# Kernel tuning notes

Hardware: AMD Instinct MI355X
Metric: run time of the kernel (lower is better)

## Reference

```python
import jax, jax.numpy as jnp
import numpy as np

B, N, D, H = 16, 1024, 384, 6
DH = D // H  # 64 per-head dim


def _layernorm(x, w, b, eps=1e-5):
    mu = jnp.mean(x, axis=-1, keepdims=True)
    var = jnp.var(x, axis=-1, keepdims=True)
    return (x - mu) * jax.lax.rsqrt(var + eps) * w + b


def setup_inputs() -> dict:
    key = jax.random.key(0)
    ks = jax.random.split(key, 10)
    std = 0.02
    return {
        "X": jax.random.normal(ks[0], (B, N, D), dtype=jnp.float32),
        "Wq": jax.random.normal(ks[1], (H, DH, D), dtype=jnp.float32) * std,
        "Wk": jax.random.normal(ks[2], (H, DH, D), dtype=jnp.float32) * std,
        "Wv": jax.random.normal(ks[3], (H, DH, D), dtype=jnp.float32) * std,
        "Wo": jax.random.normal(ks[4], (D, D), dtype=jnp.float32) * std,
        "bo": jnp.zeros((D,), dtype=jnp.float32),
        "ln1_w": jnp.ones((D,), dtype=jnp.float32),
        "ln1_b": jnp.zeros((D,), dtype=jnp.float32),
        "ln2_w": jnp.ones((D,), dtype=jnp.float32),
        "ln2_b": jnp.zeros((D,), dtype=jnp.float32),
        "W1": jax.random.normal(ks[5], (2 * D, D), dtype=jnp.float32) * std,
        "b1": jnp.zeros((2 * D,), dtype=jnp.float32),
        "W2": jax.random.normal(ks[6], (D, 2 * D), dtype=jnp.float32) * std,
        "b2": jnp.zeros((D,), dtype=jnp.float32),
    }


def reference(X, Wq, Wk, Wv, Wo, bo, ln1_w, ln1_b, ln2_w, ln2_b, W1, b1, W2, b2):
    scale = 1.0 / jnp.sqrt(jnp.float32(DH))
    # pre-LN then multi-head attention (heads vectorized, math identical to per-head loop)
    t = _layernorm(X, ln1_w, ln1_b)                       # [B,N,D]
    q = jnp.einsum('bnd,hkd->bhnk', t, Wq)                # [B,H,N,DH]
    k = jnp.einsum('bnd,hkd->bhnk', t, Wk)
    v = jnp.einsum('bnd,hkd->bhnk', t, Wv)
    scores = jnp.einsum('bhnk,bhmk->bhnm', q, k) * scale  # [B,H,N,N]
    p = jax.nn.softmax(scores, axis=-1)
    o = jnp.einsum('bhnm,bhmk->bhnk', p, v)               # [B,H,N,DH]
    o = jnp.transpose(o, (0, 2, 1, 3)).reshape(B, N, D)   # concat heads
    attn = o @ Wo.T + bo
    # residual + post-LN (dropout/drop_path are identity in eval)
    X2 = _layernorm(X + attn, ln2_w, ln2_b)
    # MLP: Linear -> exact GELU -> Linear
    h = jax.nn.gelu(X2 @ W1.T + b1, approximate=False)
    mlp = h @ W2.T + b2
    return X2 + mlp
```

## Files before the change

### kernel.cpp

```cpp
#include <hip/hip_runtime.h>
#include <math.h>

typedef float  f32x4  __attribute__((ext_vector_type(4)));
typedef __bf16 bf16x8 __attribute__((ext_vector_type(8)));
typedef __bf16 bf16x4 __attribute__((ext_vector_type(4)));

__device__ __forceinline__ void gload16(const void* g, void* l) {
  __builtin_amdgcn_global_load_lds((__attribute__((address_space(1))) const void*)g,
                                   (__attribute__((address_space(3))) void*)l, 16, 0, 0);
}

__device__ __forceinline__ f32x4 mfma16(bf16x8 a, bf16x8 b, f32x4 c) {
  return __builtin_amdgcn_mfma_f32_16x16x32_bf16(a, b, c, 0, 0, 0);
}

__global__ __launch_bounds__(256) void cvt_weights(
    const float* __restrict__ Wq, const float* __restrict__ Wk, const float* __restrict__ Wv,
    const float* __restrict__ Wo, const float* __restrict__ W1, const float* __restrict__ W2,
    __bf16* __restrict__ wqkv, __bf16* __restrict__ wo, __bf16* __restrict__ w1, __bf16* __restrict__ w2)
{
  int idx = blockIdx.x * 256 + threadIdx.x;
  if      (idx < 147456) wqkv[idx] = (__bf16)Wq[idx];
  else if (idx < 294912) wqkv[idx] = (__bf16)Wk[idx - 147456];
  else if (idx < 442368) wqkv[idx] = (__bf16)Wv[idx - 294912];
  else if (idx < 589824) wo[idx - 442368] = (__bf16)Wo[idx - 442368];
  else if (idx < 884736) w1[idx - 589824] = (__bf16)W1[idx - 589824];
  else                   w2[idx - 884736] = (__bf16)W2[idx - 884736];
}

template<int MODE>
__global__ __launch_bounds__(256) void ln_kernel(
    const float* __restrict__ in, const float* __restrict__ w, const float* __restrict__ b,
    __bf16* __restrict__ outb, float* __restrict__ outf)
{
  const int row  = blockIdx.x * 4 + (threadIdx.x >> 6);
  const int lane = threadIdx.x & 63;
  const float* x = in + (size_t)row * 384;
  float v[6]; float s = 0.f;
#pragma unroll
  for (int j = 0; j < 6; ++j) { v[j] = x[lane + 64*j]; s += v[j]; }
#pragma unroll
  for (int off = 32; off > 0; off >>= 1) s += __shfl_xor(s, off);
  const float mu = s * (1.f/384.f);
  float s2 = 0.f;
#pragma unroll
  for (int j = 0; j < 6; ++j) { float d = v[j] - mu; s2 += d*d; }
#pragma unroll
  for (int off = 32; off > 0; off >>= 1) s2 += __shfl_xor(s2, off);
  const float inv = rsqrtf(s2 * (1.f/384.f) + 1e-5f);
#pragma unroll
  for (int j = 0; j < 6; ++j) {
    const int cidx = lane + 64*j;
    const float y = (v[j]-mu)*inv*w[cidx] + b[cidx];
    outb[(size_t)row*384 + cidx] = (__bf16)y;
    if constexpr (MODE == 1) outf[(size_t)row*384 + cidx] = y;
  }
}

template<int EPI>
__global__ __launch_bounds__(256, 2) void gemm_bt(
    const __bf16* __restrict__ A, const __bf16* __restrict__ Bw,
    int M, int N, int K,
    const float* __restrict__ bias, const float* __restrict__ resid,
    float* __restrict__ outf, __bf16* __restrict__ outb,
    __bf16* __restrict__ q_out, __bf16* __restrict__ k_out, __bf16* __restrict__ vt_out)
{
  __shared__ __attribute__((aligned(16))) __bf16 As[4096];
  __shared__ __attribute__((aligned(16))) __bf16 Bs[4096];
  const int tid  = threadIdx.x;
  const int lane = tid & 63;
  const int w    = tid >> 6;
  const int wm   = w >> 1, wn = w & 1;
  const int m0   = blockIdx.y * 128, n0 = blockIdx.x * 128;

  f32x4 acc[4][4] = {};

  const __bf16* gA0 = A  + (size_t)(m0 + (w    )*16 + (lane & 15)) * K + ((lane >> 4) << 3);
  const __bf16* gA1 = A  + (size_t)(m0 + (4 + w)*16 + (lane & 15)) * K + ((lane >> 4) << 3);
  const __bf16* gB0 = Bw + (size_t)(n0 + (w    )*16 + (lane & 15)) * K + ((lane >> 4) << 3);
  const __bf16* gB1 = Bw + (size_t)(n0 + (4 + w)*16 + (lane & 15)) * K + ((lane >> 4) << 3);
  __bf16* lA0 = &As[((tid & ~63)      ) * 8];
  __bf16* lA1 = &As[((tid & ~63) + 256) * 8];
  __bf16* lB0 = &Bs[((tid & ~63)      ) * 8];
  __bf16* lB1 = &Bs[((tid & ~63) + 256) * 8];

  for (int k0 = 0; k0 < K; k0 += 32) {
    gload16(gA0 + k0, lA0);
    gload16(gA1 + k0, lA1);
    gload16(gB0 + k0, lB0);
    gload16(gB1 + k0, lB1);
    __syncthreads();
    bf16x8 af[4], bfr[4];
#pragma unroll
    for (int i = 0; i < 4; ++i) af[i]  = *(const bf16x8*)&As[(((wm*4 + i) << 6) + lane) * 8];
#pragma unroll
    for (int i = 0; i < 4; ++i) bfr[i] = *(const bf16x8*)&Bs[(((wn*4 + i) << 6) + lane) * 8];
#pragma unroll
    for (int mt = 0; mt < 4; ++mt)
#pragma unroll
      for (int nt = 0; nt < 4; ++nt)
        acc[mt][nt] = mfma16(af[mt], bfr[nt], acc[mt][nt]);
    __syncthreads();
  }

  const int quad = lane >> 4, cc = lane & 15;
#pragma unroll
  for (int mt = 0; mt < 4; ++mt) {
#pragma unroll
    for (int nt = 0; nt < 4; ++nt) {
      const int gr0 = m0 + (wm*4 + mt)*16 + quad*4;
      const int gc  = n0 + (wn*4 + nt)*16 + cc;
      f32x4 a = acc[mt][nt];
      if constexpr (EPI == 0) {
        const int bb = gr0 >> 10, nn = gr0 & 1023;
        if (gc >= 768) {
          const int jj = gc - 768, hh = jj >> 6, dh = jj & 63;
          bf16x4 pk = {(__bf16)a[0], (__bf16)a[1], (__bf16)a[2], (__bf16)a[3]};
          *(bf16x4*)&vt_out[((size_t)((bb*6 + hh)*64 + dh) << 10) + nn] = pk;
        } else {
          const bool isq = (gc < 384);
          const int jj = isq ? gc : (gc - 384);
          __bf16* dst = isq ? q_out : k_out;
          const float sc = isq ? 0.18033688011112042f : 1.0f;
          const int hh = jj >> 6, dh = jj & 63;
#pragma unroll
          for (int i = 0; i < 4; ++i)
            dst[((size_t)(((bb*6 + hh) << 10) | (nn + i)) << 6) + dh] = (__bf16)(a[i] * sc);
        }
      } else {
#pragma unroll
        for (int i = 0; i < 4; ++i) {
          const int gr = gr0 + i;
          float val = a[i];
          if constexpr (EPI == 1) {
            const size_t idx = (size_t)gr * N + gc;
            outf[idx] = val + bias[gc] + resid[idx];
          } else if constexpr (EPI == 2) {
            const float x = val + bias[gc];
            outb[(size_t)gr * N + gc] = (__bf16)(0.5f * x * (1.f + erff(x * 0.70710678118654752f)));
          } else {
            const size_t idx = (size_t)gr * N + gc;
            outf[idx] = outf[idx] + val + bias[gc];
          }
        }
      }
    }
  }
}

__global__ __launch_bounds__(256, 3) void attn_kernel(
    const __bf16* __restrict__ qp, const __bf16* __restrict__ kp,
    const __bf16* __restrict__ vtp, __bf16* __restrict__ omat)
{
  __shared__ __attribute__((aligned(16))) __bf16 Ks[4096];
  __shared__ __attribute__((aligned(16))) __bf16 Vs[4096];
  __shared__ __attribute__((aligned(16))) __bf16 Ps[4][2][1088];
  const int tid = threadIdx.x, lane = tid & 63, w = tid >> 6;
  const int bh = blockIdx.x;
  const int q0 = blockIdx.y * 128 + w * 32;
  const int quad = lane >> 4, lo = lane & 15;

  bf16x8 qa[2][2];
#pragma unroll
  for (int t = 0; t < 2; ++t) {
    const __bf16* qb = qp + ((size_t)bh * 1024 + q0 + t*16 + lo) * 64 + (quad << 3);
    qa[t][0] = *(const bf16x8*)qb;
    qa[t][1] = *(const bf16x8*)(qb + 32);
  }

  f32x4 oacc[2][4] = {};
  float l_r[2] = {0.f, 0.f};

  for (int c = 0; c < 16; ++c) {
#pragma unroll
    for (int s = 0; s < 2; ++s) {
      const int ck = s * 256 + tid;
      const int l = ck & 63, g = ck >> 6;
      const int ct = g >> 1, ks = g & 1;
      const __bf16* gk = kp + ((size_t)bh*1024 + c*64 + ct*16 + (l & 15)) * 64
                            + ks*32 + ((l >> 4) << 3);
      gload16(gk, &Ks[(ck & ~63) * 8]);
      const __bf16* gv = vtp + (((size_t)(bh*64 + ct*16 + (l & 15))) << 10)
                             + c*64 + ks*32 + ((l >> 4) << 3);
      gload16(gv, &Vs[(ck & ~63) * 8]);
    }
    __syncthreads();

    f32x4 st[2][4];
#pragma unroll
    for (int ct = 0; ct < 4; ++ct) {
      bf16x8 kb0 = *(const bf16x8*)&Ks[((ct*2 + 0)*64 + lane) * 8];
      bf16x8 kb1 = *(const bf16x8*)&Ks[((ct*2 + 1)*64 + lane) * 8];
#pragma unroll
      for (int t = 0; t < 2; ++t) {
        f32x4 s0 = {};
        s0 = mfma16(kb0, qa[t][0], s0);
        s0 = mfma16(kb1, qa[t][1], s0);
        st[t][ct] = s0;
      }
    }
#pragma unroll
    for (int t = 0; t < 2; ++t)
#pragma unroll
      for (int ct = 0; ct < 4; ++ct) {
        const float p0 = __builtin_amdgcn_exp2f(st[t][ct][0]);
        const float p1 = __builtin_amdgcn_exp2f(st[t][ct][1]);
        const float p2 = __builtin_amdgcn_exp2f(st[t][ct][2]);
        const float p3 = __builtin_amdgcn_exp2f(st[t][ct][3]);
        l_r[t] += (p0 + p1) + (p2 + p3);
        bf16x4 pk = {(__bf16)p0, (__bf16)p1, (__bf16)p2, (__bf16)p3};
        *(bf16x4*)&Ps[w][t][lo*68 + ct*16 + quad*4] = pk;
      }
    bf16x8 pa[2][2];
#pragma unroll
    for (int t = 0; t < 2; ++t)
#pragma unroll
      for (int ks = 0; ks < 2; ++ks)
        pa[t][ks] = *(const bf16x8*)&Ps[w][t][lo*68 + ks*32 + (quad << 3)];
#pragma unroll
    for (int dt = 0; dt < 4; ++dt)
#pragma unroll
      for (int ks = 0; ks < 2; ++ks) {
        bf16x8 vb = *(const bf16x8*)&Vs[((dt*2 + ks)*64 + lane) * 8];
#pragma unroll
        for (int t = 0; t < 2; ++t)
          oacc[t][dt] = mfma16(pa[t][ks], vb, oacc[t][dt]);
      }
    __syncthreads();
  }

  const int b = bh / 6, h = bh - (bh / 6) * 6;
#pragma unroll
  for (int t = 0; t < 2; ++t) {
    float ls = l_r[t];
    ls += __shfl_xor(ls, 16);
    ls += __shfl_xor(ls, 32);
#pragma unroll
    for (int i = 0; i < 4; ++i) {
      const float linv = 1.f / __shfl(ls, quad*4 + i);
      const int n = q0 + t*16 + quad*4 + i;
#pragma unroll
      for (int dt = 0; dt < 4; ++dt)
        omat[((size_t)((b << 10) | n)) * 384 + (h << 6) + dt*16 + lo] =
            (__bf16)(oacc[t][dt][i] * linv);
    }
  }
}

extern "C" void kernel_launch(void* const* d_in, const int* in_sizes, int n_in,
                              void* d_out, int out_size, void* d_ws, size_t ws_size,
                              hipStream_t stream)
{
  const float* X    = (const float*)d_in[0];
  const float* Wq   = (const float*)d_in[1];
  const float* Wk   = (const float*)d_in[2];
  const float* Wv   = (const float*)d_in[3];
  const float* Wo   = (const float*)d_in[4];
  const float* bo   = (const float*)d_in[5];
  const float* ln1w = (const float*)d_in[6];
  const float* ln1b = (const float*)d_in[7];
  const float* ln2w = (const float*)d_in[8];
  const float* ln2b = (const float*)d_in[9];
  const float* W1   = (const float*)d_in[10];
  const float* b1   = (const float*)d_in[11];
  const float* W2   = (const float*)d_in[12];
  const float* b2   = (const float*)d_in[13];

  char* ws = (char*)d_ws;
  __bf16* t_bf  = (__bf16*)(ws + 0);
  __bf16* q_bf  = (__bf16*)(ws + 12582912);
  __bf16* k_bf  = (__bf16*)(ws + 25165824);
  __bf16* omat  = (__bf16*)(ws + 37748736);
  __bf16* vt_bf = (__bf16*)(ws + 50331648);
  float*  s1    = (float*) (ws + 62914560);
  __bf16* h_bf  = (__bf16*)(ws + 62914560);
  __bf16* wqkv  = (__bf16*)(ws + 88080384);
  __bf16* wo_b  = (__bf16*)(ws + 88965120);
  __bf16* w1_b  = (__bf16*)(ws + 89260032);
  __bf16* w2_b  = (__bf16*)(ws + 89849856);
  __bf16* x2_bf = t_bf;
  float*  out   = (float*)d_out;

  cvt_weights<<<4608, 256, 0, stream>>>(Wq, Wk, Wv, Wo, W1, W2, wqkv, wo_b, w1_b, w2_b);
  ln_kernel<0><<<4096, 256, 0, stream>>>(X, ln1w, ln1b, t_bf, nullptr);
  gemm_bt<0><<<dim3(9,128), 256, 0, stream>>>(t_bf, wqkv, 16384, 1152, 384,
      nullptr, nullptr, nullptr, nullptr, q_bf, k_bf, vt_bf);
  attn_kernel<<<dim3(96,8), 256, 0, stream>>>(q_bf, k_bf, vt_bf, omat);
  gemm_bt<1><<<dim3(3,128), 256, 0, stream>>>(omat, wo_b, 16384, 384, 384,
      bo, X, s1, nullptr, nullptr, nullptr, nullptr);
  ln_kernel<1><<<4096, 256, 0, stream>>>(s1, ln2w, ln2b, x2_bf, out);
  gemm_bt<2><<<dim3(6,128), 256, 0, stream>>>(x2_bf, w1_b, 16384, 768, 384,
      b1, nullptr, nullptr, h_bf, nullptr, nullptr, nullptr);
  gemm_bt<3><<<dim3(3,128), 256, 0, stream>>>(h_bf, w2_b, 16384, 384, 768,
      b2, nullptr, out, nullptr, nullptr, nullptr, nullptr);
}
```

Measured before the change: 281.1 us.

## Double-buffer GEMM and attention LDS loads, shrink GEMM tiles, vectorize weight cast

The GEMM and attention kernels now keep two LDS buffers and issue the next K-chunk's global-to-LDS loads before computing the current one. This is meant to hide load latency behind MFMA work. The GEMM tile shrinks to 64 rows, with N tile 128 or 64 per use, and occupancy hint rises to 4, giving more blocks and better CU fill. The weight conversion kernel now handles 4 elements per thread with vector loads. The cost is more LDS per block and smaller tiles with less reuse.

```diff
diff --git a/kernel.cpp b/kernel.cpp
--- a/kernel.cpp
+++ b/kernel.cpp
@@ -19,13 +19,17 @@
     const float* __restrict__ Wo, const float* __restrict__ W1, const float* __restrict__ W2,
     __bf16* __restrict__ wqkv, __bf16* __restrict__ wo, __bf16* __restrict__ w1, __bf16* __restrict__ w2)
 {
-  int idx = blockIdx.x * 256 + threadIdx.x;
-  if      (idx < 147456) wqkv[idx] = (__bf16)Wq[idx];
-  else if (idx < 294912) wqkv[idx] = (__bf16)Wk[idx - 147456];
-  else if (idx < 442368) wqkv[idx] = (__bf16)Wv[idx - 294912];
-  else if (idx < 589824) wo[idx - 442368] = (__bf16)Wo[idx - 442368];
-  else if (idx < 884736) w1[idx - 589824] = (__bf16)W1[idx - 589824];
-  else                   w2[idx - 884736] = (__bf16)W2[idx - 884736];
+  const int idx = (blockIdx.x * 256 + threadIdx.x) * 4;
+  const float* src; __bf16* dst; int off;
+  if      (idx < 147456) { src = Wq; dst = wqkv;          off = idx; }
+  else if (idx < 294912) { src = Wk; dst = wqkv + 147456; off = idx - 147456; }
+  else if (idx < 442368) { src = Wv; dst = wqkv + 294912; off = idx - 294912; }
+  else if (idx < 589824) { src = Wo; dst = wo;            off = idx - 442368; }
+  else if (idx < 884736) { src = W1; dst = w1;            off = idx - 589824; }
+  else                   { src = W2; dst = w2;            off = idx - 884736; }
+  f32x4 v = *(const f32x4*)(src + off);
+  bf16x4 o = {(__bf16)v.x, (__bf16)v.y, (__bf16)v.z, (__bf16)v.w};
+  *(bf16x4*)(dst + off) = o;
 }
 
 template<int MODE>
@@ -57,60 +61,69 @@
   }
 }
 
-template<int EPI>
-__global__ __launch_bounds__(256, 2) void gemm_bt(
+template<int EPI, int NT>
+__global__ __launch_bounds__(256, 4) void gemm_bt(
     const __bf16* __restrict__ A, const __bf16* __restrict__ Bw,
     int M, int N, int K,
     const float* __restrict__ bias, const float* __restrict__ resid,
     float* __restrict__ outf, __bf16* __restrict__ outb,
     __bf16* __restrict__ q_out, __bf16* __restrict__ k_out, __bf16* __restrict__ vt_out)
 {
-  __shared__ __attribute__((aligned(16))) __bf16 As[4096];
-  __shared__ __attribute__((aligned(16))) __bf16 Bs[4096];
+  constexpr int CT = NT / 32;
+  __shared__ __attribute__((aligned(16))) __bf16 As[2][2048];
+  __shared__ __attribute__((aligned(16))) __bf16 Bs[2][NT * 32];
   const int tid  = threadIdx.x;
   const int lane = tid & 63;
   const int w    = tid >> 6;
   const int wm   = w >> 1, wn = w & 1;
-  const int m0   = blockIdx.y * 128, n0 = blockIdx.x * 128;
-
-  f32x4 acc[4][4] = {};
-
-  const __bf16* gA0 = A  + (size_t)(m0 + (w    )*16 + (lane & 15)) * K + ((lane >> 4) << 3);
-  const __bf16* gA1 = A  + (size_t)(m0 + (4 + w)*16 + (lane & 15)) * K + ((lane >> 4) << 3);
-  const __bf16* gB0 = Bw + (size_t)(n0 + (w    )*16 + (lane & 15)) * K + ((lane >> 4) << 3);
-  const __bf16* gB1 = Bw + (size_t)(n0 + (4 + w)*16 + (lane & 15)) * K + ((lane >> 4) << 3);
-  __bf16* lA0 = &As[((tid & ~63)      ) * 8];
-  __bf16* lA1 = &As[((tid & ~63) + 256) * 8];
-  __bf16* lB0 = &Bs[((tid & ~63)      ) * 8];
-  __bf16* lB1 = &Bs[((tid & ~63) + 256) * 8];
-
-  for (int k0 = 0; k0 < K; k0 += 32) {
-    gload16(gA0 + k0, lA0);
-    gload16(gA1 + k0, lA1);
-    gload16(gB0 + k0, lB0);
-    gload16(gB1 + k0, lB1);
+  const int m0   = blockIdx.y * 64, n0 = blockIdx.x * NT;
+
+  f32x4 acc[2][CT] = {};
+
+  const int srow = lane & 15, skq = lane >> 4;
+  const __bf16* gA  = A  + (size_t)(m0 + w*16 + srow) * K + (skq << 3);
+  const __bf16* gB0 = Bw + (size_t)(n0 + w*16 + srow) * K + (skq << 3);
+  const __bf16* gB1 = Bw + (size_t)(n0 + (4 + w)*16 + srow) * K + (skq << 3);
+  const int lbase = (tid & ~63) * 8;
+
+  auto stage = [&](int kk, int b) {
+    gload16(gA  + kk*32, &As[b][lbase]);
+    gload16(gB0 + kk*32, &Bs[b][lbase]);
+    if constexpr (NT == 128) gload16(gB1 + kk*32, &Bs[b][lbase + 2048]);
+  };
+  auto compute = [&](int b) {
+    bf16x8 af[2], bfr[CT];
+#pragma unroll
+    for (int rt = 0; rt < 2; ++rt)
+      af[rt] = *(const bf16x8*)&As[b][(((wm*2 + rt) << 6) + lane) * 8];
+#pragma unroll
+    for (int ct = 0; ct < CT; ++ct)
+      bfr[ct] = *(const bf16x8*)&Bs[b][(((wn*CT + ct) << 6) + lane) * 8];
+#pragma unroll
+    for (int rt = 0; rt < 2; ++rt)
+#pragma unroll
+      for (int ct = 0; ct < CT; ++ct)
+        acc[rt][ct] = mfma16(af[rt], bfr[ct], acc[rt][ct]);
+  };
+
+  const int NIT = K >> 5;
+  stage(0, 0);
+  __syncthreads();
+  for (int k = 0; k < NIT; ++k) {
+    const int b = k & 1;
+    if (k + 1 < NIT) stage(k + 1, b ^ 1);
+    compute(b);
     __syncthreads();
-    bf16x8 af[4], bfr[4];
-#pragma unroll
-    for (int i = 0; i < 4; ++i) af[i]  = *(const bf16x8*)&As[(((wm*4 + i) << 6) + lane) * 8];
-#pragma unroll
-    for (int i = 0; i < 4; ++i) bfr[i] = *(const bf16x8*)&Bs[(((wn*4 + i) << 6) + lane) * 8];
-#pragma unroll
-    for (int mt = 0; mt < 4; ++mt)
-#pragma unroll
-      for (int nt = 0; nt < 4; ++nt)
-        acc[mt][nt] = mfma16(af[mt], bfr[nt], acc[mt][nt]);
-    __syncthreads();
   }
 
   const int quad = lane >> 4, cc = lane & 15;
 #pragma unroll
-  for (int mt = 0; mt < 4; ++mt) {
-#pragma unroll
-    for (int nt = 0; nt < 4; ++nt) {
-      const int gr0 = m0 + (wm*4 + mt)*16 + quad*4;
-      const int gc  = n0 + (wn*4 + nt)*16 + cc;
-      f32x4 a = acc[mt][nt];
+  for (int rt = 0; rt < 2; ++rt) {
+#pragma unroll
+    for (int ct = 0; ct < CT; ++ct) {
+      const int gr0 = m0 + (wm*2 + rt)*16 + quad*4;
+      const int gc  = n0 + (wn*CT + ct)*16 + cc;
+      f32x4 a = acc[rt][ct];
       if constexpr (EPI == 0) {
         const int bb = gr0 >> 10, nn = gr0 & 1023;
         if (gc >= 768) {
@@ -152,8 +165,8 @@
     const __bf16* __restrict__ qp, const __bf16* __restrict__ kp,
     const __bf16* __restrict__ vtp, __bf16* __restrict__ omat)
 {
-  __shared__ __attribute__((aligned(16))) __bf16 Ks[4096];
-  __shared__ __attribute__((aligned(16))) __bf16 Vs[4096];
+  __shared__ __attribute__((aligned(16))) __bf16 Ks[2][4096];
+  __shared__ __attribute__((aligned(16))) __bf16 Vs[2][4096];
   __shared__ __attribute__((aligned(16))) __bf16 Ps[4][2][1088];
   const int tid = threadIdx.x, lane = tid & 63, w = tid >> 6;
   const int bh = blockIdx.x;
@@ -171,7 +184,7 @@
   f32x4 oacc[2][4] = {};
   float l_r[2] = {0.f, 0.f};
 
-  for (int c = 0; c < 16; ++c) {
+  auto stage = [&](int c, int bb) {
 #pragma unroll
     for (int s = 0; s < 2; ++s) {
       const int ck = s * 256 + tid;
@@ -179,18 +192,25 @@
       const int ct = g >> 1, ks = g & 1;
       const __bf16* gk = kp + ((size_t)bh*1024 + c*64 + ct*16 + (l & 15)) * 64
                             + ks*32 + ((l >> 4) << 3);
-      gload16(gk, &Ks[(ck & ~63) * 8]);
+      gload16(gk, &Ks[bb][(ck & ~63) * 8]);
       const __bf16* gv = vtp + (((size_t)(bh*64 + ct*16 + (l & 15))) << 10)
                              + c*64 + ks*32 + ((l >> 4) << 3);
-      gload16(gv, &Vs[(ck & ~63) * 8]);
+      gload16(gv, &Vs[bb][(ck & ~63) * 8]);
     }
-    __syncthreads();
+  };
+
+  stage(0, 0);
+  __syncthreads();
+
+  for (int c = 0; c < 16; ++c) {
+    const int bb = c & 1;
+    if (c + 1 < 16) stage(c + 1, bb ^ 1);
 
     f32x4 st[2][4];
 #pragma unroll
     for (int ct = 0; ct < 4; ++ct) {
-      bf16x8 kb0 = *(const bf16x8*)&Ks[((ct*2 + 0)*64 + lane) * 8];
-      bf16x8 kb1 = *(const bf16x8*)&Ks[((ct*2 + 1)*64 + lane) * 8];
+      bf16x8 kb0 = *(const bf16x8*)&Ks[bb][((ct*2 + 0)*64 + lane) * 8];
+      bf16x8 kb1 = *(const bf16x8*)&Ks[bb][((ct*2 + 1)*64 + lane) * 8];
 #pragma unroll
       for (int t = 0; t < 2; ++t) {
         f32x4 s0 = {};
@@ -221,7 +241,7 @@
     for (int dt = 0; dt < 4; ++dt)
 #pragma unroll
       for (int ks = 0; ks < 2; ++ks) {
-        bf16x8 vb = *(const bf16x8*)&Vs[((dt*2 + ks)*64 + lane) * 8];
+        bf16x8 vb = *(const bf16x8*)&Vs[bb][((dt*2 + ks)*64 + lane) * 8];
 #pragma unroll
         for (int t = 0; t < 2; ++t)
           oacc[t][dt] = mfma16(pa[t][ks], vb, oacc[t][dt]);
@@ -281,16 +301,16 @@
   __bf16* x2_bf = t_bf;
   float*  out   = (float*)d_out;
 
-  cvt_weights<<<4608, 256, 0, stream>>>(Wq, Wk, Wv, Wo, W1, W2, wqkv, wo_b, w1_b, w2_b);
+  cvt_weights<<<1152, 256, 0, stream>>>(Wq, Wk, Wv, Wo, W1, W2, wqkv, wo_b, w1_b, w2_b);
   ln_kernel<0><<<4096, 256, 0, stream>>>(X, ln1w, ln1b, t_bf, nullptr);
-  gemm_bt<0><<<dim3(9,128), 256, 0, stream>>>(t_bf, wqkv, 16384, 1152, 384,
+  gemm_bt<0,128><<<dim3(9,256), 256, 0, stream>>>(t_bf, wqkv, 16384, 1152, 384,
       nullptr, nullptr, nullptr, nullptr, q_bf, k_bf, vt_bf);
   attn_kernel<<<dim3(96,8), 256, 0, stream>>>(q_bf, k_bf, vt_bf, omat);
-  gemm_bt<1><<<dim3(3,128), 256, 0, stream>>>(omat, wo_b, 16384, 384, 384,
+  gemm_bt<1,64><<<dim3(6,256), 256, 0, stream>>>(omat, wo_b, 16384, 384, 384,
       bo, X, s1, nullptr, nullptr, nullptr, nullptr);
   ln_kernel<1><<<4096, 256, 0, stream>>>(s1, ln2w, ln2b, x2_bf, out);
-  gemm_bt<2><<<dim3(6,128), 256, 0, stream>>>(x2_bf, w1_b, 16384, 768, 384,
+  gemm_bt<2,128><<<dim3(6,256), 256, 0, stream>>>(x2_bf, w1_b, 16384, 768, 384,
       b1, nullptr, nullptr, h_bf, nullptr, nullptr, nullptr);
-  gemm_bt<3><<<dim3(3,128), 256, 0, stream>>>(h_bf, w2_b, 16384, 384, 768,
+  gemm_bt<3,64><<<dim3(6,256), 256, 0, stream>>>(h_bf, w2_b, 16384, 384, 768,
       b2, nullptr, out, nullptr, nullptr, nullptr, nullptr);
 }
```

After: 296.0 us. 1.05x slower.
